# Performance work log

Measured on AMD Instinct MI355X. Metric: run time of the kernel, lower is better.

The kernel has to match this reference:

```python
import jax, jax.numpy as jnp
import numpy as np

N_AGENTS = 64
_adj = np.ones((N_AGENTS, N_AGENTS)) - np.eye(N_AGENTS)
SEND_NP, RECV_NP = np.where(_adj)  # 4032 directed edges, no self-loops
N_EDGES = SEND_NP.shape[0]

D_NODE = 16
H = 64
D_OUT = 16
N_TYPES = 2
BATCH = 128


def _glorot(key, shape):
    fan_in, fan_out = shape[0], shape[1]
    lim = np.sqrt(6.0 / (fan_in + fan_out)).astype(np.float32)
    return jax.random.uniform(key, shape, jnp.float32, -lim, lim)


def setup_inputs() -> dict:
    key = jax.random.key(0)
    ks = jax.random.split(key, 16)
    inp = {
        "node_states": jax.random.normal(ks[0], (BATCH, N_AGENTS, 1, D_NODE), jnp.float32),
        "edge_types": jax.random.uniform(ks[1], (BATCH, N_EDGES, N_TYPES + 1, 1), jnp.float32),
        # edge encoder 0: MLP(32 -> 64 -> 64)
        "e0_w1": _glorot(ks[2], (2 * D_NODE, H)), "e0_b1": jnp.zeros((H,), jnp.float32),
        "e0_w2": _glorot(ks[3], (H, H)), "e0_b2": jnp.zeros((H,), jnp.float32),
        # edge encoder 1
        "e1_w1": _glorot(ks[4], (2 * D_NODE, H)), "e1_b1": jnp.zeros((H,), jnp.float32),
        "e1_w2": _glorot(ks[5], (H, H)), "e1_b2": jnp.zeros((H,), jnp.float32),
        # node decoder: MLP(16+64 -> 64 -> 16)
        "nd_w1": _glorot(ks[6], (D_NODE + H, H)), "nd_b1": jnp.zeros((H,), jnp.float32),
        "nd_w2": _glorot(ks[7], (H, D_OUT)), "nd_b2": jnp.zeros((D_OUT,), jnp.float32),
    }
    return inp


def _mlp2(x, w1, b1, w2, b2):
    h = jax.nn.relu(x @ w1 + b1)
    return jax.nn.relu(h @ w2 + b2)


def reference(node_states, edge_types,
              e0_w1, e0_b1, e0_w2, e0_b2,
              e1_w1, e1_b1, e1_w2, e1_b2,
              nd_w1, nd_b1, nd_w2, nd_b2):
    send = jnp.asarray(SEND_NP)
    recv = jnp.asarray(RECV_NP)
    # NodeAggregator: gather sender/receiver states to edges -> [B, E, 1, 2D]
    edge_msg = jnp.concatenate([node_states[:, send], node_states[:, recv]], axis=-1)
    # per-edge-type MLP encode, concat along axis 2 -> [B, E, T, H]
    enc0 = _mlp2(edge_msg, e0_w1, e0_b1, e0_w2, e0_b2)
    enc1 = _mlp2(edge_msg, e1_w1, e1_b1, e1_w2, e1_b2)
    encoded = jnp.concatenate([enc0, enc1], axis=2)
    # masked sum over edge types (skip type-0 'no edge') -> [B, E, 1, H]
    edge_msg_sum = jnp.sum(encoded * edge_types[:, :, 1:, :], axis=2, keepdims=True)
    # EdgeAggregator: scatter-sum edge messages to receiver nodes -> [B, N, 1, H]
    node_msg = jax.ops.segment_sum(
        edge_msg_sum.swapaxes(0, 1), recv, num_segments=N_AGENTS).swapaxes(0, 1)
    # decode
    node_state = jnp.concatenate([node_states, node_msg], axis=-1)  # [B, N, 1, D+H]
    return _mlp2(node_state, nd_w1, nd_b1, nd_w2, nd_b2)
```

## Files before the change

kernel.cpp:

```cpp
#include <hip/hip_runtime.h>
#include <hip/hip_fp16.h>


typedef _Float16 hf;
typedef __attribute__((ext_vector_type(8))) _Float16 v8hf;
typedef __attribute__((ext_vector_type(4))) float fv4;

union ABh { v8hf v; __half2 h[4]; };

__global__ __launch_bounds__(256, 4) void fused_kernel(
    const float* __restrict__ ns, const float* __restrict__ et,
    const float* __restrict__ e0w1, const float* __restrict__ e0b1,
    const float* __restrict__ e0w2, const float* __restrict__ e0b2,
    const float* __restrict__ e1w1, const float* __restrict__ e1b1,
    const float* __restrict__ e1w2, const float* __restrict__ e1b2,
    const float* __restrict__ ndw1, const float* __restrict__ ndb1,
    const float* __restrict__ ndw2, const float* __restrict__ ndb2,
    float* __restrict__ out)
{
  __shared__ __align__(16) _Float16 PlH[2*64*72];
  __shared__ __align__(16) _Float16 QbH[2*8*64];
  __shared__ float ETl[2*8*64];
  __shared__ __align__(16) _Float16 XDH[24*104];
  _Float16* XD  = XDH;
  _Float16* HD2 = XDH + 8*104;

  int t = threadIdx.x;
  int b = blockIdx.x >> 3, rg = blockIdx.x & 7, r0 = rg*8;
  int w = t >> 6, lane = t & 63, quad = lane >> 4, col = lane & 15;

  const __half2 z2 = __float22half2_rn(make_float2(0.f, 0.f));
  const v8hf zero8 = {};

  float xnv = 0.f;
  if (t < 128) xnv = ns[(b*64 + r0 + (t >> 4))*16 + (t & 15)];
  float ev0[2], ev1[2];
#pragma unroll
  for (int i = 0; i < 2; ++i) {
    int idx = i*256 + t;
    int s = idx >> 3, rl = idx & 7;
    int r = r0 + rl;
    float v0 = 0.f, v1 = 0.f;
    if (s != r) {
      int pos = r - (r > s ? 1 : 0);
      const float* base = et + (b*4032 + s*63 + pos)*3;
      v0 = base[1]; v1 = base[2];
    }
    ev0[i] = v0; ev1[i] = v1;
  }

  v8hf bfr[2][4][2];
  float b2v[2][4];
#pragma unroll
  for (int enc = 0; enc < 2; ++enc) {
    const float* w2 = enc ? e1w2 : e0w2;
    const float* b2 = enc ? e1b2 : e0b2;
#pragma unroll
    for (int nt = 0; nt < 4; ++nt) {
#pragma unroll
      for (int kk = 0; kk < 2; ++kk) {
        const float* base = w2 + (kk*32 + quad*8)*64 + nt*16 + col;
        ABh bb;
        bb.h[0] = __float22half2_rn(make_float2(base[0*64], base[1*64]));
        bb.h[1] = __float22half2_rn(make_float2(base[2*64], base[3*64]));
        bb.h[2] = __float22half2_rn(make_float2(base[4*64], base[5*64]));
        bb.h[3] = __float22half2_rn(make_float2(base[6*64], base[7*64]));
        bfr[enc][nt][kk] = bb.v;
      }
      b2v[enc][nt] = b2[nt*16 + col];
    }
  }

  {
    ABh a;
    if (quad < 2) {
      const float* xr = ns + (b*64 + w*16 + col)*16 + quad*8;
      float4 x0 = *(const float4*)xr;
      float4 x1 = *(const float4*)(xr + 4);
      a.h[0] = __float22half2_rn(make_float2(x0.x, x0.y));
      a.h[1] = __float22half2_rn(make_float2(x0.z, x0.w));
      a.h[2] = __float22half2_rn(make_float2(x1.x, x1.y));
      a.h[3] = __float22half2_rn(make_float2(x1.z, x1.w));
    } else {
      a.h[0] = a.h[1] = a.h[2] = a.h[3] = z2;
    }
    bool qwave = (w == (rg >> 1));
#pragma unroll 1
    for (int enc = 0; enc < 2; ++enc) {
      const float* w1 = enc ? e1w1 : e0w1;
      const float* b1 = enc ? e1b1 : e0b1;
#pragma unroll
      for (int ht = 0; ht < 4; ++ht) {
        int cc = ht*16 + col;
        ABh bb;
        if (quad < 2) {
#pragma unroll
          for (int j = 0; j < 4; ++j) {
            float f0 = w1[(quad*8 + 2*j    )*64 + cc];
            float f1 = w1[(quad*8 + 2*j + 1)*64 + cc];
            bb.h[j] = __float22half2_rn(make_float2(f0, f1));
          }
        } else {
          bb.h[0] = bb.h[1] = bb.h[2] = bb.h[3] = z2;
        }
        fv4 acc = {0.f, 0.f, 0.f, 0.f};
        acc = __builtin_amdgcn_mfma_f32_16x16x32_f16(a.v, bb.v, acc, 0, 0, 0);
        hf* pd = PlH + enc*4608 + (w*16 + quad*4)*72 + cc;
        pd[0*72] = (hf)acc[0];
        pd[1*72] = (hf)acc[1];
        pd[2*72] = (hf)acc[2];
        pd[3*72] = (hf)acc[3];
      }
      if (qwave) {
#pragma unroll
        for (int ht = 0; ht < 4; ++ht) {
          int cc = ht*16 + col;
          ABh bb;
          if (quad < 2) {
#pragma unroll
            for (int j = 0; j < 4; ++j) {
              float f0 = w1[(16 + quad*8 + 2*j    )*64 + cc];
              float f1 = w1[(16 + quad*8 + 2*j + 1)*64 + cc];
              bb.h[j] = __float22half2_rn(make_float2(f0, f1));
            }
          } else {
            bb.h[0] = bb.h[1] = bb.h[2] = bb.h[3] = z2;
          }
          fv4 acc = {0.f, 0.f, 0.f, 0.f};
          acc = __builtin_amdgcn_mfma_f32_16x16x32_f16(a.v, bb.v, acc, 0, 0, 0);
          float b1v = b1[cc];
#pragma unroll
          for (int rr = 0; rr < 4; ++rr) {
            int local = quad*4 + rr;
            if ((local >> 3) == (rg & 1))
              QbH[enc*512 + (local & 7)*64 + cc] = (hf)(acc[rr] + b1v);
          }
        }
      }
    }
  }
  if (t < 128) {
    int rl = t >> 4, k = t & 15;
    XD[rl*104 + k] = (hf)xnv;
    XD[rl*104 + 80 + k] = (hf)0.f;
  }
#pragma unroll
  for (int i = 0; i < 2; ++i) {
    int idx = i*256 + t;
    int s = idx >> 3, rl = idx & 7;
    ETl[rl*64 + s] = ev0[i];
    ETl[512 + rl*64 + s] = ev1[i];
  }
  __syncthreads();

  float msgacc[2][4] = {{0.f,0.f,0.f,0.f},{0.f,0.f,0.f,0.f}};

#pragma unroll 1
  for (int enc = 0; enc < 2; ++enc) {
#pragma unroll 1
    for (int rli = 0; rli < 2; ++rli) {
      int rl = w*2 + rli;
      const hf* qrow = QbH + (enc*8 + rl)*64;
      v8hf q0 = *(const v8hf*)(qrow + quad*8);
      v8hf q1 = *(const v8hf*)(qrow + 32 + quad*8);
      const float* etrow = ETl + (enc*8 + rl)*64;
#pragma unroll 2
      for (int st = 0; st < 4; ++st) {
        const hf* prow = PlH + enc*4608 + (st*16 + col)*72 + quad*8;
        v8hf p0 = *(const v8hf*)prow;
        v8hf p1 = *(const v8hf*)(prow + 32);
        v8hf s0 = __builtin_elementwise_max(p0 + q0, zero8);
        v8hf s1 = __builtin_elementwise_max(p1 + q1, zero8);
        float4 etv = *(const float4*)(etrow + st*16 + quad*4);
#pragma unroll
        for (int nt = 0; nt < 4; ++nt) {
          float bv = b2v[enc][nt];
          fv4 acc = {bv, bv, bv, bv};
          acc = __builtin_amdgcn_mfma_f32_16x16x32_f16(s0, bfr[enc][nt][0], acc, 0, 0, 0);
          acc = __builtin_amdgcn_mfma_f32_16x16x32_f16(s1, bfr[enc][nt][1], acc, 0, 0, 0);
          float m = msgacc[rli][nt];
          m += etv.x * fmaxf(acc[0], 0.f);
          m += etv.y * fmaxf(acc[1], 0.f);
          m += etv.z * fmaxf(acc[2], 0.f);
          m += etv.w * fmaxf(acc[3], 0.f);
          msgacc[rli][nt] = m;
        }
      }
    }
  }
#pragma unroll
  for (int rli = 0; rli < 2; ++rli) {
#pragma unroll
    for (int nt = 0; nt < 4; ++nt) {
      float v = msgacc[rli][nt];
      v += __shfl_xor(v, 16);
      v += __shfl_xor(v, 32);
      if (lane < 16) XD[(w*2 + rli)*104 + 16 + nt*16 + lane] = (hf)v;
    }
  }
  __syncthreads();

  if (w == 0) {
    ABh xa[3];
    const hf* xrow = XD + col*104;
#pragma unroll
    for (int kk = 0; kk < 3; ++kk) xa[kk].v = *(const v8hf*)(xrow + kk*32 + quad*8);
#pragma unroll
    for (int ht = 0; ht < 4; ++ht) {
      int cc = ht*16 + col;
      float bias = ndb1[cc];
      fv4 acc = {bias, bias, bias, bias};
#pragma unroll
      for (int kk = 0; kk < 3; ++kk) {
        ABh bb;
#pragma unroll
        for (int j = 0; j < 4; ++j) {
          int rA = kk*32 + quad*8 + 2*j;
          int rB = rA + 1;
          float f0 = ndw1[(rA < 80 ? rA : 79)*64 + cc] * (rA < 80 ? 1.f : 0.f);
          float f1 = ndw1[(rB < 80 ? rB : 79)*64 + cc] * (rB < 80 ? 1.f : 0.f);
          bb.h[j] = __float22half2_rn(make_float2(f0, f1));
        }
        acc = __builtin_amdgcn_mfma_f32_16x16x32_f16(xa[kk].v, bb.v, acc, 0, 0, 0);
      }
      if (quad < 2) {
#pragma unroll
        for (int rr = 0; rr < 4; ++rr)
          HD2[(quad*4 + rr)*104 + cc] = (hf)fmaxf(acc[rr], 0.f);
      }
    }
    const hf* hrow = HD2 + col*104;
    v8hf ha0 = *(const v8hf*)(hrow + quad*8);
    v8hf ha1 = *(const v8hf*)(hrow + 32 + quad*8);
    ABh b20, b21;
#pragma unroll
    for (int j = 0; j < 4; ++j) {
      float f0 = ndw2[(quad*8 + 2*j    )*16 + col];
      float f1 = ndw2[(quad*8 + 2*j + 1)*16 + col];
      b20.h[j] = __float22half2_rn(make_float2(f0, f1));
      float g0 = ndw2[(32 + quad*8 + 2*j    )*16 + col];
      float g1 = ndw2[(32 + quad*8 + 2*j + 1)*16 + col];
      b21.h[j] = __float22half2_rn(make_float2(g0, g1));
    }
    float bias2 = ndb2[col];
    fv4 acc2 = {bias2, bias2, bias2, bias2};
    acc2 = __builtin_amdgcn_mfma_f32_16x16x32_f16(ha0, b20.v, acc2, 0, 0, 0);
    acc2 = __builtin_amdgcn_mfma_f32_16x16x32_f16(ha1, b21.v, acc2, 0, 0, 0);
    if (quad < 2) {
#pragma unroll
      for (int rr = 0; rr < 4; ++rr) {
        int rl = quad*4 + rr;
        out[(b*64 + r0 + rl)*16 + col] = fmaxf(acc2[rr], 0.f);
      }
    }
  }
}

extern "C" void kernel_launch(void* const* d_in, const int* in_sizes, int n_in,
                              void* d_out, int out_size, void* d_ws, size_t ws_size,
                              hipStream_t stream) {
  const float* ns   = (const float*)d_in[0];
  const float* et   = (const float*)d_in[1];
  const float* e0w1 = (const float*)d_in[2];
  const float* e0b1 = (const float*)d_in[3];
  const float* e0w2 = (const float*)d_in[4];
  const float* e0b2 = (const float*)d_in[5];
  const float* e1w1 = (const float*)d_in[6];
  const float* e1b1 = (const float*)d_in[7];
  const float* e1w2 = (const float*)d_in[8];
  const float* e1b2 = (const float*)d_in[9];
  const float* ndw1 = (const float*)d_in[10];
  const float* ndb1 = (const float*)d_in[11];
  const float* ndw2 = (const float*)d_in[12];
  const float* ndb2 = (const float*)d_in[13];

  fused_kernel<<<1024, 256, 0, stream>>>(ns, et,
                                         e0w1, e0b1, e0w2, e0b2,
                                         e1w1, e1b1, e1w2, e1b2,
                                         ndw1, ndb1, ndw2, ndb2,
                                         (float*)d_out);
}
```

Before: 135.4 us.

## Stage encoder W1 in shared memory, split decoder layer-1 across waves, fully unroll loops

The first-layer encoder weights are loaded cooperatively with float4 reads, converted to fp16 and stored transposed in LDS, so the first MFMA stage reads B fragments with single vector LDS loads instead of strided scalar global loads. The node decoder's first layer is split so each of the four waves computes one 16-column tile instead of wave 0 doing all four, which adds an extra barrier. The encoder and message loops are fully unrolled with separate register arrays per encoder, which raises register pressure and could reduce occupancy.

```diff
diff --git a/kernel.cpp b/kernel.cpp
--- a/kernel.cpp
+++ b/kernel.cpp
@@ -18,6 +18,7 @@
     const float* __restrict__ ndw2, const float* __restrict__ ndb2,
     float* __restrict__ out)
 {
+  __shared__ __align__(16) _Float16 W1T[2*64*40 + 16];
   __shared__ __align__(16) _Float16 PlH[2*64*72];
   __shared__ __align__(16) _Float16 QbH[2*8*64];
   __shared__ float ETl[2*8*64];
@@ -48,63 +49,89 @@
     }
     ev0[i] = v0; ev1[i] = v1;
   }
-
-  v8hf bfr[2][4][2];
-  float b2v[2][4];
-#pragma unroll
-  for (int enc = 0; enc < 2; ++enc) {
-    const float* w2 = enc ? e1w2 : e0w2;
-    const float* b2 = enc ? e1b2 : e0b2;
-#pragma unroll
-    for (int nt = 0; nt < 4; ++nt) {
-#pragma unroll
-      for (int kk = 0; kk < 2; ++kk) {
-        const float* base = w2 + (kk*32 + quad*8)*64 + nt*16 + col;
-        ABh bb;
-        bb.h[0] = __float22half2_rn(make_float2(base[0*64], base[1*64]));
-        bb.h[1] = __float22half2_rn(make_float2(base[2*64], base[3*64]));
-        bb.h[2] = __float22half2_rn(make_float2(base[4*64], base[5*64]));
-        bb.h[3] = __float22half2_rn(make_float2(base[6*64], base[7*64]));
-        bfr[enc][nt][kk] = bb.v;
-      }
-      b2v[enc][nt] = b2[nt*16 + col];
-    }
-  }
+#pragma unroll
+  for (int it = 0; it < 4; ++it) {
+    int idx = it*256 + t;
+    int enc = idx >> 9, rem = idx & 511;
+    int k = rem >> 4, h0 = (rem & 15)*4;
+    const float* w1 = enc ? e1w1 : e0w1;
+    float4 v = *(const float4*)(w1 + k*64 + h0);
+    hf* dst = W1T + enc*2560 + h0*40 + k;
+    dst[0*40] = (hf)v.x; dst[1*40] = (hf)v.y; dst[2*40] = (hf)v.z; dst[3*40] = (hf)v.w;
+  }
+#pragma unroll
+  for (int d = 0; d < 4; ++d) {
+    int z = t*4 + d;
+    W1T[(z >> 3)*40 + 32 + (z & 7)] = (hf)0.f;
+  }
+  if (t < 16) W1T[5120 + t] = (hf)0.f;
+  v8hf bfr0[4][2], bfr1[4][2];
+  float b2v0[4], b2v1[4];
+#pragma unroll
+  for (int nt = 0; nt < 4; ++nt) {
+#pragma unroll
+    for (int kk = 0; kk < 2; ++kk) {
+      const float* base = e0w2 + (kk*32 + quad*8)*64 + nt*16 + col;
+      ABh bb;
+      bb.h[0] = __float22half2_rn(make_float2(base[0*64], base[1*64]));
+      bb.h[1] = __float22half2_rn(make_float2(base[2*64], base[3*64]));
+      bb.h[2] = __float22half2_rn(make_float2(base[4*64], base[5*64]));
+      bb.h[3] = __float22half2_rn(make_float2(base[6*64], base[7*64]));
+      bfr0[nt][kk] = bb.v;
+    }
+    b2v0[nt] = e0b2[nt*16 + col];
+  }
+#pragma unroll
+  for (int nt = 0; nt < 4; ++nt) {
+#pragma unroll
+    for (int kk = 0; kk < 2; ++kk) {
+      const float* base = e1w2 + (kk*32 + quad*8)*64 + nt*16 + col;
+      ABh bb;
+      bb.h[0] = __float22half2_rn(make_float2(base[0*64], base[1*64]));
+      bb.h[1] = __float22half2_rn(make_float2(base[2*64], base[3*64]));
+      bb.h[2] = __float22half2_rn(make_float2(base[4*64], base[5*64]));
+      bb.h[3] = __float22half2_rn(make_float2(base[6*64], base[7*64]));
+      bfr1[nt][kk] = bb.v;
+    }
+    b2v1[nt] = e1b2[nt*16 + col];
+  }
+  ABh a;
+  if (quad < 2) {
+    const float* xr = ns + (b*64 + w*16 + col)*16 + quad*8;
+    float4 x0 = *(const float4*)xr;
+    float4 x1 = *(const float4*)(xr + 4);
+    a.h[0] = __float22half2_rn(make_float2(x0.x, x0.y));
+    a.h[1] = __float22half2_rn(make_float2(x0.z, x0.w));
+    a.h[2] = __float22half2_rn(make_float2(x1.x, x1.y));
+    a.h[3] = __float22half2_rn(make_float2(x1.z, x1.w));
+  } else {
+    a.h[0] = a.h[1] = a.h[2] = a.h[3] = z2;
+  }
+  if (t < 128) {
+    int rl = t >> 4, k = t & 15;
+    XD[rl*104 + k] = (hf)xnv;
+    XD[rl*104 + 80 + k] = (hf)0.f;
+  }
+#pragma unroll
+  for (int i = 0; i < 2; ++i) {
+    int idx = i*256 + t;
+    int s = idx >> 3, rl = idx & 7;
+    ETl[rl*64 + s] = ev0[i];
+    ETl[512 + rl*64 + s] = ev1[i];
+  }
+  __syncthreads();
 
   {
-    ABh a;
-    if (quad < 2) {
-      const float* xr = ns + (b*64 + w*16 + col)*16 + quad*8;
-      float4 x0 = *(const float4*)xr;
-      float4 x1 = *(const float4*)(xr + 4);
-      a.h[0] = __float22half2_rn(make_float2(x0.x, x0.y));
-      a.h[1] = __float22half2_rn(make_float2(x0.z, x0.w));
-      a.h[2] = __float22half2_rn(make_float2(x1.x, x1.y));
-      a.h[3] = __float22half2_rn(make_float2(x1.z, x1.w));
-    } else {
-      a.h[0] = a.h[1] = a.h[2] = a.h[3] = z2;
-    }
     bool qwave = (w == (rg >> 1));
-#pragma unroll 1
+#pragma unroll
     for (int enc = 0; enc < 2; ++enc) {
-      const float* w1 = enc ? e1w1 : e0w1;
       const float* b1 = enc ? e1b1 : e0b1;
 #pragma unroll
       for (int ht = 0; ht < 4; ++ht) {
         int cc = ht*16 + col;
-        ABh bb;
-        if (quad < 2) {
-#pragma unroll
-          for (int j = 0; j < 4; ++j) {
-            float f0 = w1[(quad*8 + 2*j    )*64 + cc];
-            float f1 = w1[(quad*8 + 2*j + 1)*64 + cc];
-            bb.h[j] = __float22half2_rn(make_float2(f0, f1));
-          }
-        } else {
-          bb.h[0] = bb.h[1] = bb.h[2] = bb.h[3] = z2;
-        }
+        v8hf bb = *(const v8hf*)(W1T + enc*2560 + cc*40 + quad*8);
         fv4 acc = {0.f, 0.f, 0.f, 0.f};
-        acc = __builtin_amdgcn_mfma_f32_16x16x32_f16(a.v, bb.v, acc, 0, 0, 0);
+        acc = __builtin_amdgcn_mfma_f32_16x16x32_f16(a.v, bb, acc, 0, 0, 0);
         hf* pd = PlH + enc*4608 + (w*16 + quad*4)*72 + cc;
         pd[0*72] = (hf)acc[0];
         pd[1*72] = (hf)acc[1];
@@ -115,19 +142,9 @@
 #pragma unroll
         for (int ht = 0; ht < 4; ++ht) {
           int cc = ht*16 + col;
-          ABh bb;
-          if (quad < 2) {
-#pragma unroll
-            for (int j = 0; j < 4; ++j) {
-              float f0 = w1[(16 + quad*8 + 2*j    )*64 + cc];
-              float f1 = w1[(16 + quad*8 + 2*j + 1)*64 + cc];
-              bb.h[j] = __float22half2_rn(make_float2(f0, f1));
-            }
-          } else {
-            bb.h[0] = bb.h[1] = bb.h[2] = bb.h[3] = z2;
-          }
+          v8hf bb = *(const v8hf*)(W1T + enc*2560 + cc*40 + 16 + quad*8);
           fv4 acc = {0.f, 0.f, 0.f, 0.f};
-          acc = __builtin_amdgcn_mfma_f32_16x16x32_f16(a.v, bb.v, acc, 0, 0, 0);
+          acc = __builtin_amdgcn_mfma_f32_16x16x32_f16(a.v, bb, acc, 0, 0, 0);
           float b1v = b1[cc];
 #pragma unroll
           for (int rr = 0; rr < 4; ++rr) {
@@ -139,32 +156,20 @@
       }
     }
   }
-  if (t < 128) {
-    int rl = t >> 4, k = t & 15;
-    XD[rl*104 + k] = (hf)xnv;
-    XD[rl*104 + 80 + k] = (hf)0.f;
-  }
-#pragma unroll
-  for (int i = 0; i < 2; ++i) {
-    int idx = i*256 + t;
-    int s = idx >> 3, rl = idx & 7;
-    ETl[rl*64 + s] = ev0[i];
-    ETl[512 + rl*64 + s] = ev1[i];
-  }
   __syncthreads();
 
   float msgacc[2][4] = {{0.f,0.f,0.f,0.f},{0.f,0.f,0.f,0.f}};
 
-#pragma unroll 1
+#pragma unroll
   for (int enc = 0; enc < 2; ++enc) {
-#pragma unroll 1
+#pragma unroll
     for (int rli = 0; rli < 2; ++rli) {
       int rl = w*2 + rli;
       const hf* qrow = QbH + (enc*8 + rl)*64;
       v8hf q0 = *(const v8hf*)(qrow + quad*8);
       v8hf q1 = *(const v8hf*)(qrow + 32 + quad*8);
       const float* etrow = ETl + (enc*8 + rl)*64;
-#pragma unroll 2
+#pragma unroll
       for (int st = 0; st < 4; ++st) {
         const hf* prow = PlH + enc*4608 + (st*16 + col)*72 + quad*8;
         v8hf p0 = *(const v8hf*)prow;
@@ -174,10 +179,10 @@
         float4 etv = *(const float4*)(etrow + st*16 + quad*4);
 #pragma unroll
         for (int nt = 0; nt < 4; ++nt) {
-          float bv = b2v[enc][nt];
+          float bv = enc ? b2v1[nt] : b2v0[nt];
           fv4 acc = {bv, bv, bv, bv};
-          acc = __builtin_amdgcn_mfma_f32_16x16x32_f16(s0, bfr[enc][nt][0], acc, 0, 0, 0);
-          acc = __builtin_amdgcn_mfma_f32_16x16x32_f16(s1, bfr[enc][nt][1], acc, 0, 0, 0);
+          acc = __builtin_amdgcn_mfma_f32_16x16x32_f16(s0, enc ? bfr1[nt][0] : bfr0[nt][0], acc, 0, 0, 0);
+          acc = __builtin_amdgcn_mfma_f32_16x16x32_f16(s1, enc ? bfr1[nt][1] : bfr0[nt][1], acc, 0, 0, 0);
           float m = msgacc[rli][nt];
           m += etv.x * fmaxf(acc[0], 0.f);
           m += etv.y * fmaxf(acc[1], 0.f);
@@ -200,35 +205,35 @@
   }
   __syncthreads();
 
-  if (w == 0) {
+  {
     ABh xa[3];
     const hf* xrow = XD + col*104;
 #pragma unroll
     for (int kk = 0; kk < 3; ++kk) xa[kk].v = *(const v8hf*)(xrow + kk*32 + quad*8);
-#pragma unroll
-    for (int ht = 0; ht < 4; ++ht) {
-      int cc = ht*16 + col;
-      float bias = ndb1[cc];
-      fv4 acc = {bias, bias, bias, bias};
-#pragma unroll
-      for (int kk = 0; kk < 3; ++kk) {
-        ABh bb;
-#pragma unroll
-        for (int j = 0; j < 4; ++j) {
-          int rA = kk*32 + quad*8 + 2*j;
-          int rB = rA + 1;
-          float f0 = ndw1[(rA < 80 ? rA : 79)*64 + cc] * (rA < 80 ? 1.f : 0.f);
-          float f1 = ndw1[(rB < 80 ? rB : 79)*64 + cc] * (rB < 80 ? 1.f : 0.f);
-          bb.h[j] = __float22half2_rn(make_float2(f0, f1));
-        }
-        acc = __builtin_amdgcn_mfma_f32_16x16x32_f16(xa[kk].v, bb.v, acc, 0, 0, 0);
-      }
-      if (quad < 2) {
-#pragma unroll
-        for (int rr = 0; rr < 4; ++rr)
-          HD2[(quad*4 + rr)*104 + cc] = (hf)fmaxf(acc[rr], 0.f);
-      }
-    }
+    int cc = w*16 + col;
+    float bias = ndb1[cc];
+    fv4 acc = {bias, bias, bias, bias};
+#pragma unroll
+    for (int kk = 0; kk < 3; ++kk) {
+      ABh bb;
+#pragma unroll
+      for (int j = 0; j < 4; ++j) {
+        int rA = kk*32 + quad*8 + 2*j, rB = rA + 1;
+        float f0 = (rA < 80) ? ndw1[rA*64 + cc] : 0.f;
+        float f1 = (rB < 80) ? ndw1[rB*64 + cc] : 0.f;
+        bb.h[j] = __float22half2_rn(make_float2(f0, f1));
+      }
+      acc = __builtin_amdgcn_mfma_f32_16x16x32_f16(xa[kk].v, bb.v, acc, 0, 0, 0);
+    }
+    if (quad < 2) {
+#pragma unroll
+      for (int rr = 0; rr < 4; ++rr)
+        HD2[(quad*4 + rr)*104 + cc] = (hf)fmaxf(acc[rr], 0.f);
+    }
+  }
+  __syncthreads();
+
+  if (w == 0) {
     const hf* hrow = HD2 + col*104;
     v8hf ha0 = *(const v8hf*)(hrow + quad*8);
     v8hf ha1 = *(const v8hf*)(hrow + 32 + quad*8);
```

New measurement: 269.3 us. 98.9% more time.
